# Optimization experiments

Measured on AMD Instinct MI355X. Metric: run time of the kernel, lower is better.

Reference implementation:

```python
import jax, jax.numpy as jnp
import numpy as np

N_NODES = 100000
N_EDGES = 1600000
IN_DIM = 128
HID = 64      # gat_hidden
HEADS = 4
D = HID // HEADS  # per-head out_dim = 16
EPS = 1e-9
NEG_SLOPE = 0.2


def setup_inputs() -> dict:
    key = jax.random.key(0)
    ks = jax.random.split(key, 10)
    x = jax.random.normal(ks[0], (N_NODES, IN_DIM), dtype=jnp.float32)
    edge_index = jax.random.randint(ks[1], (2, N_EDGES), 0, N_NODES, dtype=jnp.int32)
    # node_embed: Linear(IN_DIM, HID) + ReLU (dropout = identity in eval)
    w_embed = jax.random.normal(ks[2], (IN_DIM, HID), dtype=jnp.float32) * 0.08
    b_embed = jnp.zeros((HID,), dtype=jnp.float32)
    # two GAT layers: lin (HID -> HEADS*D, no bias), att_src/att_dst [HEADS, D]
    lin_w0 = jax.random.normal(ks[3], (HID, HEADS * D), dtype=jnp.float32) * 0.12
    att_src0 = jax.random.normal(ks[4], (HEADS, D), dtype=jnp.float32) * 0.25
    att_dst0 = jax.random.normal(ks[5], (HEADS, D), dtype=jnp.float32) * 0.25
    lin_w1 = jax.random.normal(ks[6], (HID, HEADS * D), dtype=jnp.float32) * 0.12
    att_src1 = jax.random.normal(ks[7], (HEADS, D), dtype=jnp.float32) * 0.25
    att_dst1 = jax.random.normal(ks[8], (HEADS, D), dtype=jnp.float32) * 0.25
    return {
        "x": x, "w_embed": w_embed, "b_embed": b_embed,
        "lin_w0": lin_w0, "att_src0": att_src0, "att_dst0": att_dst0,
        "lin_w1": lin_w1, "att_src1": att_src1, "att_dst1": att_dst1,
        "edge_index": edge_index,
    }


def _gat_layer(h, src, dst, lin_w, att_src, att_dst):
    # h: [N, HID] -> out: [N, HEADS*D]
    n = h.shape[0]
    xp = (h @ lin_w).reshape(n, HEADS, D)          # [N, H, D]
    x_j = xp[src]                                   # source (neighbor) feats [E, H, D]
    x_i = xp[dst]                                   # destination feats      [E, H, D]
    e = (x_j * att_src).sum(-1) + (x_i * att_dst).sum(-1)   # [E, H]
    e = jnp.where(e > 0, e, NEG_SLOPE * e)          # LeakyReLU(0.2)
    exp_e = jnp.exp(e)                              # unnormalized, matches original (no max-subtract)
    denom = jax.ops.segment_sum(exp_e, dst, num_segments=n)  # [N, H]
    alpha = exp_e / (denom[dst] + EPS)              # [E, H]
    out = jax.ops.segment_sum(x_j * alpha[:, :, None], dst, num_segments=n)  # [N, H, D]
    return out.reshape(n, HEADS * D)


def reference(x, w_embed, b_embed, lin_w0, att_src0, att_dst0,
              lin_w1, att_src1, att_dst1, edge_index):
    src, dst = edge_index[0], edge_index[1]
    h = jax.nn.relu(x @ w_embed + b_embed)          # node_embed (eval: dropout = id)
    h = _gat_layer(h, src, dst, lin_w0, att_src0, att_dst0)
    h = _gat_layer(h, src, dst, lin_w1, att_src1, att_dst1)
    return jax.nn.relu(h)                            # gat_post (eval)
```

## Files before the change

kernel.cpp:

```cpp
#include <hip/hip_runtime.h>
#include <hip/hip_bf16.h>

#define N_HEADS 4
#define HID 64
#define IN_DIM 128
#define EPS 1e-9f
#define NEG_SLOPE 0.2f
#define CAP 48
#define NRANGE 8

typedef int   v4i __attribute__((ext_vector_type(4)));
typedef float v4f __attribute__((ext_vector_type(4)));

__device__ __forceinline__ void linatt_phase(
        const float (*hs)[HID], int base,
        const float* __restrict__ lw,
        const float* __restrict__ att_s, const float* __restrict__ att_d,
        __hip_bfloat16* __restrict__ xpb, float* __restrict__ asrc,
        float* __restrict__ adst, int N) {
    int wv = threadIdx.x >> 6;
    int j  = threadIdx.x & 63;
    int n0 = base + wv * 4;
    float acc[4] = {0.f, 0.f, 0.f, 0.f};
    const float (*hr)[HID] = &hs[wv * 4];
    #pragma unroll 2
    for (int k = 0; k < HID; k += 4) {
        float4 h0v = *(const float4*)(&hr[0][k]);
        float4 h1v = *(const float4*)(&hr[1][k]);
        float4 h2v = *(const float4*)(&hr[2][k]);
        float4 h3v = *(const float4*)(&hr[3][k]);
        float w0 = lw[(k + 0) * HID + j];
        float w1 = lw[(k + 1) * HID + j];
        float w2 = lw[(k + 2) * HID + j];
        float w3 = lw[(k + 3) * HID + j];
        acc[0] = fmaf(h0v.x, w0, acc[0]); acc[0] = fmaf(h0v.y, w1, acc[0]);
        acc[0] = fmaf(h0v.z, w2, acc[0]); acc[0] = fmaf(h0v.w, w3, acc[0]);
        acc[1] = fmaf(h1v.x, w0, acc[1]); acc[1] = fmaf(h1v.y, w1, acc[1]);
        acc[1] = fmaf(h1v.z, w2, acc[1]); acc[1] = fmaf(h1v.w, w3, acc[1]);
        acc[2] = fmaf(h2v.x, w0, acc[2]); acc[2] = fmaf(h2v.y, w1, acc[2]);
        acc[2] = fmaf(h2v.z, w2, acc[2]); acc[2] = fmaf(h2v.w, w3, acc[2]);
        acc[3] = fmaf(h3v.x, w0, acc[3]); acc[3] = fmaf(h3v.y, w1, acc[3]);
        acc[3] = fmaf(h3v.z, w2, acc[3]); acc[3] = fmaf(h3v.w, w3, acc[3]);
    }
    float as = att_s[j], adw = att_d[j];
    #pragma unroll
    for (int q = 0; q < 4; ++q) {
        if (n0 + q >= N) break;
        float a = acc[q];
        xpb[(size_t)(n0 + q) * HID + j] = __float2bfloat16(a);
        float vs = a * as;
        float vd = a * adw;
        #pragma unroll
        for (int off = 8; off > 0; off >>= 1) {
            vs += __shfl_down(vs, off, 16);
            vd += __shfl_down(vd, off, 16);
        }
        if ((j & 15) == 0) {
            asrc[(size_t)(n0 + q) * N_HEADS + (j >> 4)] = vs;
            adst[(size_t)(n0 + q) * N_HEADS + (j >> 4)] = vd;
        }
    }
}

__global__ void __launch_bounds__(256) scatter_embed_kernel(
        const int* __restrict__ src, const int* __restrict__ dst,
        int* __restrict__ cnt, int* __restrict__ csr, int E, int N,
        const float* __restrict__ x, const float* __restrict__ w,
        const float* __restrict__ b, const float* __restrict__ lw,
        const float* __restrict__ att_s, const float* __restrict__ att_d,
        __hip_bfloat16* __restrict__ xpb, float* __restrict__ asrc,
        float* __restrict__ adst) {
    __shared__ float xs[16][IN_DIM];
    __shared__ float hs[16][HID];
    int B = blockIdx.x;
    int m = B % 24;
    if (m % 3 != 2) {
        int r = B & 7;
        int occ = (0x6D9200u >> m) & 1;
        int seq = (B / 24) * 2 + occ;
        int i4 = seq * 256 + (int)threadIdx.x;
        int range = (N + NRANGE - 1) / NRANGE;
        int lo = r * range;
        int hi = lo + range; hi = hi < N ? hi : N;
        int nq = E >> 2;
        if (i4 >= nq) return;
        int4 d4 = ((const int4*)dst)[i4];
        int ebase = i4 * 4;
        int dd[4] = {d4.x, d4.y, d4.z, d4.w};
        #pragma unroll
        for (int q = 0; q < 4; ++q) {
            int d = dd[q];
            if (d >= lo && d < hi) {
                int p = atomicAdd(&cnt[d], 1);
                if (p < CAP) csr[(size_t)d * CAP + p] = src[ebase + q];
            }
        }
        return;
    }
    int eidx = B / 3;
    int base = eidx * 16;
    if (base >= N) return;
    int wv = threadIdx.x >> 6;
    int j  = threadIdx.x & 63;
    const v4f* xg = (const v4f*)(x + ((size_t)base + wv * 4) * IN_DIM);
    #pragma unroll
    for (int i = 0; i < 2; ++i) {
        int f4 = i * 64 + j;
        int row = f4 >> 5;
        int nn = base + wv * 4 + row;
        v4f v = (nn < N) ? xg[f4] : (v4f)0.f;
        *((v4f*)&xs[wv * 4 + row][(f4 & 31) * 4]) = v;
    }
    {
        float acc[4] = {0.f, 0.f, 0.f, 0.f};
        const float (*xr)[IN_DIM] = &xs[wv * 4];
        #pragma unroll 2
        for (int k = 0; k < IN_DIM; k += 4) {
            float4 v0 = *(const float4*)(&xr[0][k]);
            float4 v1 = *(const float4*)(&xr[1][k]);
            float4 v2 = *(const float4*)(&xr[2][k]);
            float4 v3 = *(const float4*)(&xr[3][k]);
            float w0 = w[(k + 0) * HID + j];
            float w1 = w[(k + 1) * HID + j];
            float w2 = w[(k + 2) * HID + j];
            float w3 = w[(k + 3) * HID + j];
            acc[0] = fmaf(v0.x, w0, acc[0]); acc[0] = fmaf(v0.y, w1, acc[0]);
            acc[0] = fmaf(v0.z, w2, acc[0]); acc[0] = fmaf(v0.w, w3, acc[0]);
            acc[1] = fmaf(v1.x, w0, acc[1]); acc[1] = fmaf(v1.y, w1, acc[1]);
            acc[1] = fmaf(v1.z, w2, acc[1]); acc[1] = fmaf(v1.w, w3, acc[1]);
            acc[2] = fmaf(v2.x, w0, acc[2]); acc[2] = fmaf(v2.y, w1, acc[2]);
            acc[2] = fmaf(v2.z, w2, acc[2]); acc[2] = fmaf(v2.w, w3, acc[2]);
            acc[3] = fmaf(v3.x, w0, acc[3]); acc[3] = fmaf(v3.y, w1, acc[3]);
            acc[3] = fmaf(v3.z, w2, acc[3]); acc[3] = fmaf(v3.w, w3, acc[3]);
        }
        float bb = b[j];
        #pragma unroll
        for (int q = 0; q < 4; ++q)
            hs[wv * 4 + q][j] = fmaxf(acc[q] + bb, 0.f);
    }
    linatt_phase(hs, base, lw, att_s, att_d, xpb, asrc, adst, N);
}

template <int WRITE_LDS>
__device__ __forceinline__ void agg_octet(
        int base, int N,
        const int* __restrict__ cnt, const int* __restrict__ csr,
        const float* __restrict__ asrc, const float* __restrict__ adst,
        const __hip_bfloat16* __restrict__ xpb,
        float (*hs)[HID], float* __restrict__ out) {
    int wv = threadIdx.x >> 6;
    int lane = threadIdx.x & 63;
    int eg = lane >> 2, hh = lane & 3;
    int k4 = (lane >> 3) << 2;
    int b  = lane & 7;
    int kb4H = k4 + (b >> 1);

    #pragma unroll
    for (int rr = 0; rr < 4; ++rr) {
        int nid = base + wv * 4 + rr;
        int node = nid < N ? nid : N - 1;
        int deg = cnt[node];
        deg = deg < CAP ? deg : CAP;
        if (nid >= N) deg = 0;
        const int* bucket = csr + (size_t)node * CAP;
        float adA = adst[(unsigned)node * N_HEADS + (unsigned)hh];
        int ng = (deg + 15) >> 4;
        float acc[8] = {0.f, 0.f, 0.f, 0.f, 0.f, 0.f, 0.f, 0.f};
        float wsum = 0.f;
        for (int g = 0; g < ng; ++g) {
            int t = g * 16 + eg;
            int raw = bucket[t];
            unsigned s = (t < deg) ? (unsigned)raw : 0u;
            float e = asrc[s * N_HEADS + (unsigned)hh] + adA;
            e = fmaxf(e, NEG_SLOPE * e);
            float w = (t < deg) ? __expf(e) : 0.f;
            #pragma unroll
            for (int p = 0; p < 2; ++p) {
                unsigned s_k = (unsigned)__shfl((int)s, k4 + p * 32, 64);
                float    w_k = __shfl(w, kb4H + p * 32, 64);
                uint4 v = *(const uint4*)(xpb + (size_t)s_k * HID + b * 8);
                acc[0] = fmaf(w_k, __uint_as_float(v.x << 16),          acc[0]);
                acc[1] = fmaf(w_k, __uint_as_float(v.x & 0xffff0000u),  acc[1]);
                acc[2] = fmaf(w_k, __uint_as_float(v.y << 16),          acc[2]);
                acc[3] = fmaf(w_k, __uint_as_float(v.y & 0xffff0000u),  acc[3]);
                acc[4] = fmaf(w_k, __uint_as_float(v.z << 16),          acc[4]);
                acc[5] = fmaf(w_k, __uint_as_float(v.z & 0xffff0000u),  acc[5]);
                acc[6] = fmaf(w_k, __uint_as_float(v.w << 16),          acc[6]);
                acc[7] = fmaf(w_k, __uint_as_float(v.w & 0xffff0000u),  acc[7]);
                wsum += w_k;
            }
        }
        #pragma unroll
        for (int i = 0; i < 8; ++i) acc[i] += __shfl_down(acc[i], 8, 64);
        wsum += __shfl_down(wsum, 8, 64);
        #pragma unroll
        for (int i = 0; i < 8; ++i) acc[i] += __shfl_down(acc[i], 16, 64);
        wsum += __shfl_down(wsum, 16, 64);
        #pragma unroll
        for (int i = 0; i < 8; ++i) acc[i] += __shfl_down(acc[i], 32, 64);
        wsum += __shfl_down(wsum, 32, 64);

        if (lane < 8 && nid < N) {
            float inv = 1.f / (wsum + EPS);
            if (WRITE_LDS) {
                v4f lo = {acc[0] * inv, acc[1] * inv, acc[2] * inv, acc[3] * inv};
                v4f hi = {acc[4] * inv, acc[5] * inv, acc[6] * inv, acc[7] * inv};
                *((v4f*)&hs[wv * 4 + rr][lane * 8])     = lo;
                *((v4f*)&hs[wv * 4 + rr][lane * 8 + 4]) = hi;
            } else {
                float* op = out + (size_t)nid * HID + lane * 8;
                v4f lo = {fmaxf(acc[0] * inv, 0.f), fmaxf(acc[1] * inv, 0.f),
                          fmaxf(acc[2] * inv, 0.f), fmaxf(acc[3] * inv, 0.f)};
                v4f hi = {fmaxf(acc[4] * inv, 0.f), fmaxf(acc[5] * inv, 0.f),
                          fmaxf(acc[6] * inv, 0.f), fmaxf(acc[7] * inv, 0.f)};
                *(v4f*)op = lo;
                *(v4f*)(op + 4) = hi;
            }
        }
    }
}

__global__ void __launch_bounds__(256) agg_linatt_kernel(
        const int* __restrict__ cnt, const int* __restrict__ csr,
        const float* __restrict__ asrc0, const float* __restrict__ adst0,
        const __hip_bfloat16* __restrict__ xpb0,
        const float* __restrict__ lw, const float* __restrict__ att_s,
        const float* __restrict__ att_d,
        __hip_bfloat16* __restrict__ xpb1, float* __restrict__ asrc1,
        float* __restrict__ adst1, int N) {
    __shared__ float hs[16][HID];
    int base = blockIdx.x * 16;
    agg_octet<1>(base, N, cnt, csr, asrc0, adst0, xpb0, hs, nullptr);
    linatt_phase(hs, base, lw, att_s, att_d, xpb1, asrc1, adst1, N);
}

__global__ void __launch_bounds__(256) agg_kernel(
        const int* __restrict__ cnt, const int* __restrict__ csr,
        const float* __restrict__ asrc, const float* __restrict__ adst,
        const __hip_bfloat16* __restrict__ xpb, float* __restrict__ out, int N) {
    int base = blockIdx.x * 16;
    agg_octet<0>(base, N, cnt, csr, asrc, adst, xpb, nullptr, out);
}

extern "C" void kernel_launch(void* const* d_in, const int* in_sizes, int n_in,
                              void* d_out, int out_size, void* d_ws, size_t ws_size,
                              hipStream_t stream) {
    const float* x       = (const float*)d_in[0];
    const float* w_embed = (const float*)d_in[1];
    const float* b_embed = (const float*)d_in[2];
    const float* lin_w0  = (const float*)d_in[3];
    const float* att_s0  = (const float*)d_in[4];
    const float* att_d0  = (const float*)d_in[5];
    const float* lin_w1  = (const float*)d_in[6];
    const float* att_s1  = (const float*)d_in[7];
    const float* att_d1  = (const float*)d_in[8];
    const int*   ei      = (const int*)d_in[9];

    const int N = in_sizes[0] / IN_DIM;
    const int E = in_sizes[9] / 2;
    const int* src = ei;
    const int* dst = ei + E;

    float* ws    = (float*)d_ws;
    float* asrc0 = ws;
    float* adst0 = asrc0 + (size_t)N * N_HEADS;
    float* asrc1 = adst0 + (size_t)N * N_HEADS;
    float* adst1 = asrc1 + (size_t)N * N_HEADS;
    int*   cnt   = (int*)(adst1 + (size_t)N * N_HEADS);
    int*   csr   = cnt + N;
    __hip_bfloat16* xpb0 = (__hip_bfloat16*)(csr + (size_t)N * CAP);
    __hip_bfloat16* xpb1 = xpb0 + (size_t)N * HID;
    float* outp = (float*)d_out;

    int blk16 = (N + 15) / 16;
    int nq = E >> 2;
    int seqs = (nq + 255) / 256;
    int g_sc = (seqs + 1) / 2;
    int g_em = (blk16 + 7) / 8;
    int groups = g_sc > g_em ? g_sc : g_em;
    int fused_blocks = groups * 24;

    hipMemsetAsync(cnt, 0, (size_t)N * sizeof(int), stream);

    scatter_embed_kernel<<<fused_blocks, 256, 0, stream>>>(
        src, dst, cnt, csr, E, N,
        x, w_embed, b_embed, lin_w0, att_s0, att_d0, xpb0, asrc0, adst0);

    agg_linatt_kernel<<<blk16, 256, 0, stream>>>(
        cnt, csr, asrc0, adst0, xpb0, lin_w1, att_s1, att_d1, xpb1, asrc1, adst1, N);

    agg_kernel<<<blk16, 256, 0, stream>>>(cnt, csr, asrc1, adst1, xpb1, outp, N);
}
```

Before: 208.1 us.

## Stage embed and linear weights in LDS, vectorize src loads in scatter

```diff
diff --git a/kernel.cpp b/kernel.cpp
--- a/kernel.cpp
+++ b/kernel.cpp
@@ -14,7 +14,7 @@
 
 __device__ __forceinline__ void linatt_phase(
         const float (*hs)[HID], int base,
-        const float* __restrict__ lw,
+        const float* lw,
         const float* __restrict__ att_s, const float* __restrict__ att_d,
         __hip_bfloat16* __restrict__ xpb, float* __restrict__ asrc,
         float* __restrict__ adst, int N) {
@@ -70,6 +70,7 @@
         const float* __restrict__ att_s, const float* __restrict__ att_d,
         __hip_bfloat16* __restrict__ xpb, float* __restrict__ asrc,
         float* __restrict__ adst) {
+    __shared__ float ws_lds[64][HID];
     __shared__ float xs[16][IN_DIM];
     __shared__ float hs[16][HID];
     int B = blockIdx.x;
@@ -85,14 +86,15 @@
         int nq = E >> 2;
         if (i4 >= nq) return;
         int4 d4 = ((const int4*)dst)[i4];
-        int ebase = i4 * 4;
+        int4 s4 = ((const int4*)src)[i4];
         int dd[4] = {d4.x, d4.y, d4.z, d4.w};
+        int ss[4] = {s4.x, s4.y, s4.z, s4.w};
         #pragma unroll
         for (int q = 0; q < 4; ++q) {
             int d = dd[q];
             if (d >= lo && d < hi) {
                 int p = atomicAdd(&cnt[d], 1);
-                if (p < CAP) csr[(size_t)d * CAP + p] = src[ebase + q];
+                if (p < CAP) csr[(size_t)d * CAP + p] = ss[q];
             }
         }
         return;
@@ -111,19 +113,27 @@
         v4f v = (nn < N) ? xg[f4] : (v4f)0.f;
         *((v4f*)&xs[wv * 4 + row][(f4 & 31) * 4]) = v;
     }
-    {
-        float acc[4] = {0.f, 0.f, 0.f, 0.f};
-        const float (*xr)[IN_DIM] = &xs[wv * 4];
+    float acc[4] = {0.f, 0.f, 0.f, 0.f};
+    const float (*xr)[IN_DIM] = &xs[wv * 4];
+    #pragma unroll
+    for (int half = 0; half < 2; ++half) {
+        __syncthreads();
+        const v4f* wg = (const v4f*)(w + (size_t)half * 64 * HID);
+        #pragma unroll
+        for (int i = 0; i < 4; ++i)
+            ((v4f*)ws_lds)[i * 256 + threadIdx.x] = wg[i * 256 + threadIdx.x];
+        __syncthreads();
         #pragma unroll 2
-        for (int k = 0; k < IN_DIM; k += 4) {
-            float4 v0 = *(const float4*)(&xr[0][k]);
-            float4 v1 = *(const float4*)(&xr[1][k]);
-            float4 v2 = *(const float4*)(&xr[2][k]);
-            float4 v3 = *(const float4*)(&xr[3][k]);
-            float w0 = w[(k + 0) * HID + j];
-            float w1 = w[(k + 1) * HID + j];
-            float w2 = w[(k + 2) * HID + j];
-            float w3 = w[(k + 3) * HID + j];
+        for (int k = 0; k < 64; k += 4) {
+            int kk = half * 64 + k;
+            float4 v0 = *(const float4*)(&xr[0][kk]);
+            float4 v1 = *(const float4*)(&xr[1][kk]);
+            float4 v2 = *(const float4*)(&xr[2][kk]);
+            float4 v3 = *(const float4*)(&xr[3][kk]);
+            float w0 = ws_lds[k + 0][j];
+            float w1 = ws_lds[k + 1][j];
+            float w2 = ws_lds[k + 2][j];
+            float w3 = ws_lds[k + 3][j];
             acc[0] = fmaf(v0.x, w0, acc[0]); acc[0] = fmaf(v0.y, w1, acc[0]);
             acc[0] = fmaf(v0.z, w2, acc[0]); acc[0] = fmaf(v0.w, w3, acc[0]);
             acc[1] = fmaf(v1.x, w0, acc[1]); acc[1] = fmaf(v1.y, w1, acc[1]);
@@ -133,11 +143,11 @@
             acc[3] = fmaf(v3.x, w0, acc[3]); acc[3] = fmaf(v3.y, w1, acc[3]);
             acc[3] = fmaf(v3.z, w2, acc[3]); acc[3] = fmaf(v3.w, w3, acc[3]);
         }
-        float bb = b[j];
-        #pragma unroll
-        for (int q = 0; q < 4; ++q)
-            hs[wv * 4 + q][j] = fmaxf(acc[q] + bb, 0.f);
-    }
+    }
+    float bb = b[j];
+    #pragma unroll
+    for (int q = 0; q < 4; ++q)
+        hs[wv * 4 + q][j] = fmaxf(acc[q] + bb, 0.f);
     linatt_phase(hs, base, lw, att_s, att_d, xpb, asrc, adst, N);
 }
 
@@ -229,9 +239,14 @@
         __hip_bfloat16* __restrict__ xpb1, float* __restrict__ asrc1,
         float* __restrict__ adst1, int N) {
     __shared__ float hs[16][HID];
+    __shared__ float lw_s[HID][HID];
     int base = blockIdx.x * 16;
+    #pragma unroll
+    for (int i = 0; i < 4; ++i)
+        ((v4f*)lw_s)[i * 256 + threadIdx.x] = ((const v4f*)lw)[i * 256 + threadIdx.x];
     agg_octet<1>(base, N, cnt, csr, asrc0, adst0, xpb0, hs, nullptr);
-    linatt_phase(hs, base, lw, att_s, att_d, xpb1, asrc1, adst1, N);
+    __syncthreads();
+    linatt_phase(hs, base, &lw_s[0][0], att_s, att_d, xpb1, asrc1, adst1, N);
 }
 
 __global__ void __launch_bounds__(256) agg_kernel(
```

Result: slower. 219.8 us (+5.7%).

## Rebalance fused scatter/embed blocks and stage layer-1 weights in LDS

Applied to the files above, without the earlier changes.

```diff
diff --git a/kernel.cpp b/kernel.cpp
--- a/kernel.cpp
+++ b/kernel.cpp
@@ -14,7 +14,7 @@
 
 __device__ __forceinline__ void linatt_phase(
         const float (*hs)[HID], int base,
-        const float* __restrict__ lw,
+        const float* lw,
         const float* __restrict__ att_s, const float* __restrict__ att_d,
         __hip_bfloat16* __restrict__ xpb, float* __restrict__ asrc,
         float* __restrict__ adst, int N) {
@@ -74,30 +74,38 @@
     __shared__ float hs[16][HID];
     int B = blockIdx.x;
     int m = B % 24;
-    if (m % 3 != 2) {
-        int r = B & 7;
-        int occ = (0x6D9200u >> m) & 1;
-        int seq = (B / 24) * 2 + occ;
-        int i4 = seq * 256 + (int)threadIdx.x;
+    int g = B / 24;
+    if (m % 3 == 2) {
+        int r = m & 7;
         int range = (N + NRANGE - 1) / NRANGE;
         int lo = r * range;
         int hi = lo + range; hi = hi < N ? hi : N;
         int nq = E >> 2;
-        if (i4 >= nq) return;
-        int4 d4 = ((const int4*)dst)[i4];
-        int ebase = i4 * 4;
-        int dd[4] = {d4.x, d4.y, d4.z, d4.w};
-        #pragma unroll
-        for (int q = 0; q < 4; ++q) {
-            int d = dd[q];
-            if (d >= lo && d < hi) {
-                int p = atomicAdd(&cnt[d], 1);
-                if (p < CAP) csr[(size_t)d * CAP + p] = src[ebase + q];
+        int tid = threadIdx.x;
+        int4 d4v[4], s4v[4];
+        #pragma unroll
+        for (int k = 0; k < 4; ++k) {
+            int i4 = g * 1024 + k * 256 + tid;
+            bool ok = i4 < nq;
+            d4v[k] = ok ? ((const int4*)dst)[i4] : make_int4(-1, -1, -1, -1);
+            s4v[k] = ok ? ((const int4*)src)[i4] : make_int4(0, 0, 0, 0);
+        }
+        #pragma unroll
+        for (int k = 0; k < 4; ++k) {
+            int dd[4] = {d4v[k].x, d4v[k].y, d4v[k].z, d4v[k].w};
+            int ss[4] = {s4v[k].x, s4v[k].y, s4v[k].z, s4v[k].w};
+            #pragma unroll
+            for (int q = 0; q < 4; ++q) {
+                int d = dd[q];
+                if (d >= lo && d < hi) {
+                    int p = atomicAdd(&cnt[d], 1);
+                    if (p < CAP) csr[(size_t)d * CAP + p] = ss[q];
+                }
             }
         }
         return;
     }
-    int eidx = B / 3;
+    int eidx = g * 16 + (m - m / 3);
     int base = eidx * 16;
     if (base >= N) return;
     int wv = threadIdx.x >> 6;
@@ -229,9 +237,14 @@
         __hip_bfloat16* __restrict__ xpb1, float* __restrict__ asrc1,
         float* __restrict__ adst1, int N) {
     __shared__ float hs[16][HID];
+    __shared__ float lw_s[HID][HID];
     int base = blockIdx.x * 16;
+    #pragma unroll
+    for (int i = 0; i < 4; ++i)
+        ((v4f*)lw_s)[i * 256 + threadIdx.x] = ((const v4f*)lw)[i * 256 + threadIdx.x];
     agg_octet<1>(base, N, cnt, csr, asrc0, adst0, xpb0, hs, nullptr);
-    linatt_phase(hs, base, lw, att_s, att_d, xpb1, asrc1, adst1, N);
+    __syncthreads();
+    linatt_phase(hs, base, &lw_s[0][0], att_s, att_d, xpb1, asrc1, adst1, N);
 }
 
 __global__ void __launch_bounds__(256) agg_kernel(
@@ -274,9 +287,8 @@
 
     int blk16 = (N + 15) / 16;
     int nq = E >> 2;
-    int seqs = (nq + 255) / 256;
-    int g_sc = (seqs + 1) / 2;
-    int g_em = (blk16 + 7) / 8;
+    int g_sc = (nq + 1023) / 1024;
+    int g_em = (blk16 + 15) / 16;
     int groups = g_sc > g_em ? g_sc : g_em;
     int fused_blocks = groups * 24;
 
```

New measurement: 212.2 us. No clear change (+2.0%).
